# Optimization experiments

Hardware: AMD Instinct MI355X
Metric: run time of the kernel (lower is better)

Reference implementation:

```python
import jax, jax.numpy as jnp
import numpy as np

B, C, H, W = 8, 256, 128, 128

def setup_inputs() -> dict:
    key = jax.random.key(0)
    k1, k2 = jax.random.split(key)
    x = jax.random.normal(k1, (B, C, H, W), dtype=jnp.float32)
    # guide is a per-pixel gate map (broadcast over channels), values in [0, 1)
    guide = jax.random.uniform(k2, (B, 1, H, W), dtype=jnp.float32)
    return {"x": x, "guide": guide}

def reference(x, guide):
    # guide.expand_as(x): broadcast the [B,1,H,W] gate over channels
    g = jnp.broadcast_to(guide, x.shape)
    gated = x * g  # guide-modulated features
    # Guided directional max pool: running max along W (left -> right),
    # i.e. out[..., t] = max_{j <= t} (x * guide)[..., j].
    # associative_scan with jnp.maximum is the exact, differentiable cummax;
    # the argmax index ('maxout' in the CUDA op) is implicit in autodiff.
    out = jax.lax.associative_scan(jnp.maximum, gated, axis=-1)
    return out
```

## Files before the change

kernel.cpp:

```cpp
#include <hip/hip_runtime.h>

#define PB 8
#define PC 256
#define PH 128
#define PW 128
#define TOTAL_ROWS (PB * PC * PH)
#define ROWS_PER_THREAD 4
#define ROW_GROUPS (TOTAL_ROWS / ROWS_PER_THREAD)

typedef float vfloat4 __attribute__((ext_vector_type(4)));

__global__ __launch_bounds__(256, 8) void i5pool_cummax_kernel(
    const float* __restrict__ x,
    const float* __restrict__ guide,
    float* __restrict__ out)
{
    const int tid = blockIdx.x * blockDim.x + threadIdx.x;
    const int sub = tid & 31;
    const int rg  = tid >> 5;

    const int h = rg & (PH - 1);
    const int g = rg >> 7;
    const int b = rg >> 13;

    const size_t row0  = ((size_t)(g << 2)) * PH + h;
    const size_t xoff  = row0 * PW + sub * 4;
    const size_t goff  = ((size_t)b * PH + h) * PW + sub * 4;

    const vfloat4* xp = (const vfloat4*)(x + xoff);
    vfloat4*       op = (vfloat4*)(out + xoff);
    const size_t kstride = (size_t)PH * PW / 4;

    vfloat4 xv[ROWS_PER_THREAD];
    #pragma unroll
    for (int k = 0; k < ROWS_PER_THREAD; ++k)
        xv[k] = __builtin_nontemporal_load(xp + k * kstride);
    const vfloat4 gv = *(const vfloat4*)(guide + goff);

    vfloat4 ov[ROWS_PER_THREAD];
    float  tot[ROWS_PER_THREAD];
    #pragma unroll
    for (int k = 0; k < ROWS_PER_THREAD; ++k) {
        float e0 = xv[k].x * gv.x;
        float e1 = fmaxf(e0, xv[k].y * gv.y);
        float e2 = fmaxf(e1, xv[k].z * gv.z);
        float e3 = fmaxf(e2, xv[k].w * gv.w);
        ov[k].x = e0; ov[k].y = e1; ov[k].z = e2; ov[k].w = e3;
        tot[k] = e3;
    }

    #pragma unroll
    for (int d = 1; d < 32; d <<= 1) {
        float t0 = __shfl_up(tot[0], d, 32);
        float t1 = __shfl_up(tot[1], d, 32);
        float t2 = __shfl_up(tot[2], d, 32);
        float t3 = __shfl_up(tot[3], d, 32);
        tot[0] = fmaxf(tot[0], t0);
        tot[1] = fmaxf(tot[1], t1);
        tot[2] = fmaxf(tot[2], t2);
        tot[3] = fmaxf(tot[3], t3);
    }

    #pragma unroll
    for (int k = 0; k < ROWS_PER_THREAD; ++k) {
        float pre = __shfl_up(tot[k], 1, 32);
        if (sub == 0) pre = -__builtin_inff();
        ov[k].x = fmaxf(ov[k].x, pre);
        ov[k].y = fmaxf(ov[k].y, pre);
        ov[k].z = fmaxf(ov[k].z, pre);
        ov[k].w = fmaxf(ov[k].w, pre);
    }

    #pragma unroll
    for (int k = 0; k < ROWS_PER_THREAD; ++k)
        __builtin_nontemporal_store(ov[k], op + k * kstride);
}

extern "C" void kernel_launch(void* const* d_in, const int* in_sizes, int n_in,
                              void* d_out, int out_size, void* d_ws, size_t ws_size,
                              hipStream_t stream) {
    const float* x     = (const float*)d_in[0];
    const float* guide = (const float*)d_in[1];
    float* out = (float*)d_out;

    const int total_threads = ROW_GROUPS * 32;
    const int block = 256;
    const int grid = total_threads / block;

    i5pool_cummax_kernel<<<grid, block, 0, stream>>>(x, guide, out);
}
```

Baseline: 219.8 us.

## Switch to persistent grid-stride rows with double-buffered register prefetch

The kernel used to launch one thread group per four rows, with the guide loaded once for those four channel rows. It now launches a fixed grid of 2048 blocks that stride over rows, keeping two row segments in registers so the next segment's loads are issued while the current one is scanned and stored. The aim is to hide memory latency through software pipelining and fewer, longer-lived blocks. In exchange the guide row is reloaded for every row instead of shared across four channels, and the launch-bounds occupancy hint is dropped.

```diff
diff --git a/kernel.cpp b/kernel.cpp
--- a/kernel.cpp
+++ b/kernel.cpp
@@ -5,75 +5,84 @@
 #define PH 128
 #define PW 128
 #define TOTAL_ROWS (PB * PC * PH)
-#define ROWS_PER_THREAD 4
-#define ROW_GROUPS (TOTAL_ROWS / ROWS_PER_THREAD)
+#define NBLK 2048
+#define BLOCK 256
+#define SEGS_PER_BLOCK (BLOCK / 32)
+#define NITER (TOTAL_ROWS / (NBLK * SEGS_PER_BLOCK))
 
 typedef float vfloat4 __attribute__((ext_vector_type(4)));
 
-__global__ __launch_bounds__(256, 8) void i5pool_cummax_kernel(
+struct Seg {
+    vfloat4 xv;
+    vfloat4 gv;
+};
+
+__device__ __forceinline__ void seg_load(Seg& s, const float* __restrict__ x,
+                                         const float* __restrict__ guide,
+                                         int row, int sub)
+{
+    const int h = row & (PH - 1);
+    const int b = row >> 15;
+    const size_t xoff = (size_t)row * PW + sub * 4;
+    const size_t goff = (((size_t)b << 7) + h) * PW + sub * 4;
+    s.xv = __builtin_nontemporal_load((const vfloat4*)(x + xoff));
+    s.gv = *(const vfloat4*)(guide + goff);
+}
+
+__device__ __forceinline__ void seg_cs(const Seg& s, float* __restrict__ out,
+                                       int row, int sub)
+{
+    float e0 = s.xv.x * s.gv.x;
+    float e1 = fmaxf(e0, s.xv.y * s.gv.y);
+    float e2 = fmaxf(e1, s.xv.z * s.gv.z);
+    float e3 = fmaxf(e2, s.xv.w * s.gv.w);
+
+    float t = e3;
+    #pragma unroll
+    for (int d = 1; d < 32; d <<= 1) {
+        float u = __shfl_up(t, d, 32);
+        t = fmaxf(t, u);
+    }
+    float pre = __shfl_up(t, 1, 32);
+    if (sub == 0) pre = -__builtin_inff();
+
+    vfloat4 ov;
+    ov.x = fmaxf(e0, pre);
+    ov.y = fmaxf(e1, pre);
+    ov.z = fmaxf(e2, pre);
+    ov.w = fmaxf(e3, pre);
+
+    const size_t xoff = (size_t)row * PW + sub * 4;
+    __builtin_nontemporal_store(ov, (vfloat4*)(out + xoff));
+}
+
+__global__ __launch_bounds__(BLOCK) void i5pool_cummax_kernel(
     const float* __restrict__ x,
     const float* __restrict__ guide,
     float* __restrict__ out)
 {
-    const int tid = blockIdx.x * blockDim.x + threadIdx.x;
-    const int sub = tid & 31;
-    const int rg  = tid >> 5;
+    const int sub = threadIdx.x & 31;
+    const int seg = threadIdx.x >> 5;
+    const int bl  = blockIdx.x;
 
-    const int h = rg & (PH - 1);
-    const int g = rg >> 7;
-    const int b = rg >> 13;
+    const int rbase = bl * SEGS_PER_BLOCK + seg;
+    const int rstep = NBLK * SEGS_PER_BLOCK;
 
-    const size_t row0  = ((size_t)(g << 2)) * PH + h;
-    const size_t xoff  = row0 * PW + sub * 4;
-    const size_t goff  = ((size_t)b * PH + h) * PW + sub * 4;
-
-    const vfloat4* xp = (const vfloat4*)(x + xoff);
-    vfloat4*       op = (vfloat4*)(out + xoff);
-    const size_t kstride = (size_t)PH * PW / 4;
-
-    vfloat4 xv[ROWS_PER_THREAD];
-    #pragma unroll
-    for (int k = 0; k < ROWS_PER_THREAD; ++k)
-        xv[k] = __builtin_nontemporal_load(xp + k * kstride);
-    const vfloat4 gv = *(const vfloat4*)(guide + goff);
-
-    vfloat4 ov[ROWS_PER_THREAD];
-    float  tot[ROWS_PER_THREAD];
-    #pragma unroll
-    for (int k = 0; k < ROWS_PER_THREAD; ++k) {
-        float e0 = xv[k].x * gv.x;
-        float e1 = fmaxf(e0, xv[k].y * gv.y);
-        float e2 = fmaxf(e1, xv[k].z * gv.z);
-        float e3 = fmaxf(e2, xv[k].w * gv.w);
-        ov[k].x = e0; ov[k].y = e1; ov[k].z = e2; ov[k].w = e3;
-        tot[k] = e3;
-    }
+    Seg A, B;
+    seg_load(A, x, guide, rbase,         sub);
+    seg_load(B, x, guide, rbase + rstep, sub);
 
     #pragma unroll
-    for (int d = 1; d < 32; d <<= 1) {
-        float t0 = __shfl_up(tot[0], d, 32);
-        float t1 = __shfl_up(tot[1], d, 32);
-        float t2 = __shfl_up(tot[2], d, 32);
-        float t3 = __shfl_up(tot[3], d, 32);
-        tot[0] = fmaxf(tot[0], t0);
-        tot[1] = fmaxf(tot[1], t1);
-        tot[2] = fmaxf(tot[2], t2);
-        tot[3] = fmaxf(tot[3], t3);
+    for (int it = 0; it < NITER / 2 - 1; ++it) {
+        const int r0 = rbase + (2 * it) * rstep;
+        seg_cs(A, out, r0, sub);
+        seg_load(A, x, guide, r0 + 2 * rstep, sub);
+        seg_cs(B, out, r0 + rstep, sub);
+        seg_load(B, x, guide, r0 + 3 * rstep, sub);
     }
-
-    #pragma unroll
-    for (int k = 0; k < ROWS_PER_THREAD; ++k) {
-        float pre = __shfl_up(tot[k], 1, 32);
-        if (sub == 0) pre = -__builtin_inff();
-        ov[k].x = fmaxf(ov[k].x, pre);
-        ov[k].y = fmaxf(ov[k].y, pre);
-        ov[k].z = fmaxf(ov[k].z, pre);
-        ov[k].w = fmaxf(ov[k].w, pre);
-    }
-
-    #pragma unroll
-    for (int k = 0; k < ROWS_PER_THREAD; ++k)
-        __builtin_nontemporal_store(ov[k], op + k * kstride);
+    const int rl = rbase + (NITER - 2) * rstep;
+    seg_cs(A, out, rl, sub);
+    seg_cs(B, out, rl + rstep, sub);
 }
 
 extern "C" void kernel_launch(void* const* d_in, const int* in_sizes, int n_in,
@@ -83,9 +92,5 @@
     const float* guide = (const float*)d_in[1];
     float* out = (float*)d_out;
 
-    const int total_threads = ROW_GROUPS * 32;
-    const int block = 256;
-    const int grid = total_threads / block;
-
-    i5pool_cummax_kernel<<<grid, block, 0, stream>>>(x, guide, out);
+    i5pool_cummax_kernel<<<NBLK, BLOCK, 0, stream>>>(x, guide, out);
 }
```

New measurement: 226.2 us. 2.9% more time.
